# Kernel tuning notes

Measured on AMD Instinct MI355X. Metric: run time of the kernel, lower is better.

## Reference

```python
import jax, jax.numpy as jnp
import numpy as np

N_NODES = 100000
N_EDGES = 3200000
IN_FEAT = 128


def gcn_conv(x, src, dst, W, b, num_nodes):
    # PyG GCNConv: h = x @ W, then symmetric-normalized aggregation with self-loops.
    h = x @ W  # [N, out]
    # add self loops
    loop = jnp.arange(num_nodes, dtype=src.dtype)
    s = jnp.concatenate([src, loop])
    d = jnp.concatenate([dst, loop])
    # degree over destination (col) with unit edge weights
    deg = jax.ops.segment_sum(jnp.ones_like(s, dtype=h.dtype), d, num_segments=num_nodes)
    dinv = jnp.where(deg > 0, jax.lax.rsqrt(deg), 0.0)
    norm = dinv[s] * dinv[d]  # [E+N]
    msg = norm[:, None] * h[s]  # gather source features, scale per edge
    out = jax.ops.segment_sum(msg, d, num_segments=num_nodes)
    return out + b


def setup_inputs() -> dict:
    key = jax.random.key(0)
    ks = jax.random.split(key, 8)
    x = jax.random.normal(ks[0], (N_NODES, IN_FEAT), dtype=jnp.float32)
    edge_index = jax.random.randint(ks[1], (2, N_EDGES), 0, N_NODES, dtype=jnp.int64)
    def glorot(k, shape):
        lim = np.sqrt(6.0 / (shape[0] + shape[1]))
        return jax.random.uniform(k, shape, jnp.float32, -lim, lim)
    return {
        "x": x,
        "edge_index": edge_index,
        "W1": glorot(ks[2], (IN_FEAT, 4)), "b1": jnp.zeros((4,), jnp.float32),
        "W2": glorot(ks[3], (4, 2)),       "b2": jnp.zeros((2,), jnp.float32),
        "W3": glorot(ks[4], (2, 1)),       "b3": jnp.zeros((1,), jnp.float32),
    }


def reference(x, edge_index, W1, b1, W2, b2, W3, b3):
    src, dst = edge_index[0], edge_index[1]
    n = x.shape[0]
    h = gcn_conv(x, src, dst, W1, b1, n)
    h = jax.nn.relu(h)
    # F.dropout(training=self.training): inference mode -> identity
    h = gcn_conv(h, src, dst, W2, b2, n)
    h = jax.nn.relu(h)
    h = gcn_conv(h, src, dst, W3, b3, n)
    return jax.nn.sigmoid(h)  # [N, 1]
```

## Files before the change

kernel.cpp:

```cpp
#include <hip/hip_runtime.h>
#include <math.h>


#define TPB 256
#define CHUNK 4096
#define EPT (CHUNK / TPB)
#define BSZ 128
#define SLAB2 4992
#define NSMAX 1024

__global__ __launch_bounds__(TPB) void k_part(
    const int* __restrict__ src, const int* __restrict__ dst,
    unsigned int* __restrict__ slab, int* __restrict__ lstartT,
    const float* __restrict__ x, const float* __restrict__ W1,
    float* __restrict__ h1,
    int NB, int NS, int E, int N)
{
    __shared__ int hist[NSMAX];
    __shared__ unsigned int sorted[CHUNK];
    __shared__ int wtot[4];
    int t = threadIdx.x;

    if (blockIdx.x >= NS) {
        float* Ws = (float*)sorted;
        for (int i = t; i < 512; i += TPB) Ws[i] = W1[i];
        __syncthreads();
        int tt = (blockIdx.x - NS) * TPB + t;
        int v = tt >> 2, p = tt & 3;
        if (v >= N) return;
        const float4* xr = (const float4*)(x + (size_t)v * 128);
        float a0 = 0.f, a1 = 0.f, a2 = 0.f, a3 = 0.f;
#pragma unroll
        for (int i = 0; i < 8; ++i) {
            int cc = p + i * 4;
            float4 xx = xr[cc];
            const float* wv = &Ws[cc * 16];
            a0 += xx.x*wv[0] + xx.y*wv[4] + xx.z*wv[8]  + xx.w*wv[12];
            a1 += xx.x*wv[1] + xx.y*wv[5] + xx.z*wv[9]  + xx.w*wv[13];
            a2 += xx.x*wv[2] + xx.y*wv[6] + xx.z*wv[10] + xx.w*wv[14];
            a3 += xx.x*wv[3] + xx.y*wv[7] + xx.z*wv[11] + xx.w*wv[15];
        }
        a0 += __shfl_xor(a0,1); a0 += __shfl_xor(a0,2);
        a1 += __shfl_xor(a1,1); a1 += __shfl_xor(a1,2);
        a2 += __shfl_xor(a2,1); a2 += __shfl_xor(a2,2);
        a3 += __shfl_xor(a3,1); a3 += __shfl_xor(a3,2);
        if (p == 0) ((float4*)h1)[v] = make_float4(a0, a1, a2, a3);
        return;
    }

    int base = blockIdx.x * CHUNK;
    int n = min(CHUNK, E - base);
    for (int i = t; i < NSMAX; i += TPB) hist[i] = 0;
    __syncthreads();
    unsigned int meta[EPT];
#pragma unroll
    for (int k = 0; k < EPT; ++k) {
        int li = k * TPB + t;
        if (li < n) {
            int d = dst[base + li];
            int lp = atomicAdd(&hist[d >> 7], 1);
            meta[k] = ((unsigned)d << 13) | (unsigned)lp;
        } else meta[k] = 0xFFFFFFFFu;
    }
    __syncthreads();
    int lane = t & 63, w = t >> 6;
    int q0 = hist[4*t], q1 = hist[4*t+1], q2 = hist[4*t+2], q3 = hist[4*t+3];
    int pq = q0 + q1 + q2 + q3, xs = pq;
    for (int d = 1; d < 64; d <<= 1) { int y = __shfl_up(xs, d); if (lane >= d) xs += y; }
    if (lane == 63) wtot[w] = xs;
    __syncthreads();
    int woff = 0;
#pragma unroll
    for (int i = 0; i < 4; ++i) if (i < w) woff += wtot[i];
    int e0 = woff + xs - pq;
    hist[4*t]   = e0;
    hist[4*t+1] = e0 + q0;
    hist[4*t+2] = e0 + q0 + q1;
    hist[4*t+3] = e0 + q0 + q1 + q2;
    __syncthreads();
#pragma unroll
    for (int k = 0; k < EPT; ++k) {
        if (meta[k] != 0xFFFFFFFFu) {
            unsigned m = meta[k];
            int d = (int)(m >> 13);
            int lp = (int)(m & 0x1FFFu);
            unsigned pk = (unsigned)src[base + k*TPB + t] | ((unsigned)(d & 127) << 17);
            sorted[hist[d >> 7] + lp] = pk;
        }
    }
    __syncthreads();
    const uint4* s4 = (const uint4*)sorted;
    uint4* g4 = (uint4*)(slab + (size_t)base);
    for (int i = t; i < CHUNK / 4; i += TPB) g4[i] = s4[i];
    for (int i = t; i < NB + 1; i += TPB)
        lstartT[(size_t)i * NS + blockIdx.x] = hist[i];
}

__global__ __launch_bounds__(TPB) void k_degree(
    const unsigned int* __restrict__ slab, const int* __restrict__ lstartT,
    int* __restrict__ ssrc, int2* __restrict__ oc, float* __restrict__ dinv,
    const float* __restrict__ h1, float* __restrict__ hs1,
    int NS, int NB, int N)
{
    __shared__ unsigned int pl[SLAB2];
    __shared__ int sstart[NSMAX];
    __shared__ int slen[NSMAX];
    __shared__ int c[BSZ];
    __shared__ int cur[BSZ];
    __shared__ int wtot[4];
    int t = threadIdx.x, b = blockIdx.x;
    if (t < BSZ) c[t] = 0;
    for (int j = t; j < NSMAX; j += TPB) {
        int st = 0, len = 0;
        if (j < NS) {
            st  = lstartT[(size_t)b * NS + j];
            len = lstartT[(size_t)(b + 1) * NS + j] - st;
        }
        sstart[j] = st;
        slen[j] = len;
    }
    __syncthreads();
    int lane = t & 63, w = t >> 6;
    int s0 = slen[4*t], s1 = slen[4*t+1], s2 = slen[4*t+2], s3 = slen[4*t+3];
    int pq = s0 + s1 + s2 + s3, xs = pq;
    for (int d = 1; d < 64; d <<= 1) { int y = __shfl_up(xs, d); if (lane >= d) xs += y; }
    if (lane == 63) wtot[w] = xs;
    __syncthreads();
    int woff = 0, tot = 0;
#pragma unroll
    for (int i = 0; i < 4; ++i) { int z = wtot[i]; tot += z; if (i < w) woff += z; }
    int e0 = woff + xs - pq;
    slen[4*t]   = e0;
    slen[4*t+1] = e0 + s0;
    slen[4*t+2] = e0 + s0 + s1;
    slen[4*t+3] = e0 + s0 + s1 + s2;
    __syncthreads();
    int total = min(tot, SLAB2);
    for (int i = t; i < total; i += TPB) {
        int lo = 0, hi = NS;
        while (hi - lo > 1) {
            int mid = (lo + hi) >> 1;
            bool le = (slen[mid] <= i);
            lo = le ? mid : lo;
            hi = le ? hi : mid;
        }
        pl[i] = slab[(size_t)lo * CHUNK + sstart[lo] + (i - slen[lo])];
    }
    __syncthreads();
    for (int i = t; i < total; i += TPB) atomicAdd(&c[(pl[i] >> 17) & 127], 1);
    __syncthreads();
    int cv = (t < BSZ) ? c[t] : 0;
    int xc = cv;
    for (int d = 1; d < 64; d <<= 1) { int y = __shfl_up(xc, d); if (lane >= d) xc += y; }
    if (lane == 63) wtot[w] = xc;
    __syncthreads();
    int woff2 = 0;
#pragma unroll
    for (int i = 0; i < 4; ++i) if (i < w) woff2 += wtot[i];
    int excl = woff2 + xc - cv;
    if (t < BSZ) {
        int v = (b << 7) + t;
        if (v < N) {
            oc[v] = make_int2(b * SLAB2 + excl, cv);
            float di = rsqrtf((float)(cv + 1));
            dinv[v] = di;
            float4 hv = ((const float4*)h1)[v];
            ((float4*)hs1)[v] = make_float4(di*hv.x, di*hv.y, di*hv.z, di*hv.w);
        }
        cur[t] = excl;
    }
    __syncthreads();
    int* sb = ssrc + (size_t)b * SLAB2;
    for (int i = t; i < total; i += TPB) {
        unsigned pk = pl[i];
        int pos = atomicAdd(&cur[(pk >> 17) & 127], 1);
        sb[pos] = (int)(pk & 0x1FFFFu);
    }
}

__global__ __launch_bounds__(TPB) void k_gather1(
    const int2* __restrict__ oc, const int* __restrict__ ssrc,
    const float* __restrict__ hs1, const float* __restrict__ dinv,
    const float* __restrict__ b1, const float* __restrict__ W2,
    float* __restrict__ hs2, int n) {
    int t = blockIdx.x * TPB + threadIdx.x;
    int v = t >> 3, p = t & 7;
    if (v >= n) return;
    int2 ocv = oc[v];
    int base = ocv.x, c = ocv.y;
    float4 acc = make_float4(0.f, 0.f, 0.f, 0.f);
    for (int i = p; i < c; i += 8) {
        int s = ssrc[base + i];
        float4 h = ((const float4*)hs1)[s];
        acc.x += h.x; acc.y += h.y; acc.z += h.z; acc.w += h.w;
    }
    acc.x += __shfl_xor(acc.x, 1); acc.x += __shfl_xor(acc.x, 2); acc.x += __shfl_xor(acc.x, 4);
    acc.y += __shfl_xor(acc.y, 1); acc.y += __shfl_xor(acc.y, 2); acc.y += __shfl_xor(acc.y, 4);
    acc.z += __shfl_xor(acc.z, 1); acc.z += __shfl_xor(acc.z, 2); acc.z += __shfl_xor(acc.z, 4);
    acc.w += __shfl_xor(acc.w, 1); acc.w += __shfl_xor(acc.w, 2); acc.w += __shfl_xor(acc.w, 4);
    if (p == 0) {
        float4 hv = ((const float4*)hs1)[v];
        float di = dinv[v];
        float o0 = fmaxf(di * (acc.x + hv.x) + b1[0], 0.f);
        float o1 = fmaxf(di * (acc.y + hv.y) + b1[1], 0.f);
        float o2 = fmaxf(di * (acc.z + hv.z) + b1[2], 0.f);
        float o3 = fmaxf(di * (acc.w + hv.w) + b1[3], 0.f);
        float g0 = o0 * W2[0] + o1 * W2[2] + o2 * W2[4] + o3 * W2[6];
        float g1 = o0 * W2[1] + o1 * W2[3] + o2 * W2[5] + o3 * W2[7];
        ((float2*)hs2)[v] = make_float2(di * g0, di * g1);
    }
}

__global__ __launch_bounds__(TPB) void k_gather2(
    const int2* __restrict__ oc, const int* __restrict__ ssrc,
    const float* __restrict__ hs2, const float* __restrict__ dinv,
    const float* __restrict__ b2, const float* __restrict__ W3,
    float* __restrict__ hs3, int n) {
    int t = blockIdx.x * TPB + threadIdx.x;
    int v = t >> 3, p = t & 7;
    if (v >= n) return;
    int2 ocv = oc[v];
    int base = ocv.x, c = ocv.y;
    float2 acc = make_float2(0.f, 0.f);
    for (int i = p; i < c; i += 8) {
        int s = ssrc[base + i];
        float2 h = ((const float2*)hs2)[s];
        acc.x += h.x; acc.y += h.y;
    }
    acc.x += __shfl_xor(acc.x, 1); acc.x += __shfl_xor(acc.x, 2); acc.x += __shfl_xor(acc.x, 4);
    acc.y += __shfl_xor(acc.y, 1); acc.y += __shfl_xor(acc.y, 2); acc.y += __shfl_xor(acc.y, 4);
    if (p == 0) {
        float2 hv = ((const float2*)hs2)[v];
        float di = dinv[v];
        float o0 = fmaxf(di * (acc.x + hv.x) + b2[0], 0.f);
        float o1 = fmaxf(di * (acc.y + hv.y) + b2[1], 0.f);
        float h3 = o0 * W3[0] + o1 * W3[1];
        hs3[v] = di * h3;
    }
}

__global__ __launch_bounds__(TPB) void k_gather3(
    const int2* __restrict__ oc, const int* __restrict__ ssrc,
    const float* __restrict__ hs3, const float* __restrict__ dinv,
    const float* __restrict__ b3, float* __restrict__ out, int n) {
    int t = blockIdx.x * TPB + threadIdx.x;
    int v = t >> 3, p = t & 7;
    if (v >= n) return;
    int2 ocv = oc[v];
    int base = ocv.x, c = ocv.y;
    float acc = 0.f;
    for (int i = p; i < c; i += 8) acc += hs3[ssrc[base + i]];
    acc += __shfl_xor(acc, 1); acc += __shfl_xor(acc, 2); acc += __shfl_xor(acc, 4);
    if (p == 0) {
        float di = dinv[v];
        float agg = di * (acc + hs3[v]) + b3[0];
        out[v] = 1.0f / (1.0f + __expf(-agg));
    }
}

extern "C" void kernel_launch(void* const* d_in, const int* in_sizes, int n_in,
                              void* d_out, int out_size, void* d_ws, size_t ws_size,
                              hipStream_t stream) {
    const float* x  = (const float*)d_in[0];
    const int* ei   = (const int*)d_in[1];
    const float* W1 = (const float*)d_in[2];
    const float* b1 = (const float*)d_in[3];
    const float* W2 = (const float*)d_in[4];
    const float* b2 = (const float*)d_in[5];
    const float* W3 = (const float*)d_in[6];
    const float* b3 = (const float*)d_in[7];
    float* out = (float*)d_out;

    const int N = in_sizes[0] / 128;
    const int E = in_sizes[1] / 2;
    const int* src = ei;
    const int* dst = ei + E;

    const int NS = (E + CHUNK - 1) / CHUNK;
    const int NB = (N + BSZ - 1) / BSZ;

    char* w = (char*)d_ws;
    auto carve = [&](size_t bytes) { char* p = w; w += (bytes + 15) & ~(size_t)15; return p; };
    unsigned int* slab = (unsigned int*)carve((size_t)NS * CHUNK * 4);
    int* lstartT       = (int*)carve((size_t)(NB + 1) * NS * 4);
    int* ssrc          = (int*)carve((size_t)NB * SLAB2 * 4);
    int2* oc           = (int2*)carve((size_t)N * 8);
    float* dinv        = (float*)carve((size_t)N * 4);
    float* h1          = (float*)carve((size_t)4 * N * 4);
    float* hs1         = (float*)carve((size_t)4 * N * 4);
    float* hs2         = (float*)carve((size_t)2 * N * 4);
    float* hs3         = (float*)carve((size_t)N * 4);

    const int nb1  = (4 * N + TPB - 1) / TPB;
    const int nbN8 = (8 * N + TPB - 1) / TPB;

    k_part   <<<NS + nb1, TPB, 0, stream>>>(src, dst, slab, lstartT, x, W1, h1, NB, NS, E, N);
    k_degree <<<NB, TPB, 0, stream>>>(slab, lstartT, ssrc, oc, dinv, h1, hs1, NS, NB, N);
    k_gather1<<<nbN8, TPB, 0, stream>>>(oc, ssrc, hs1, dinv, b1, W2, hs2, N);
    k_gather2<<<nbN8, TPB, 0, stream>>>(oc, ssrc, hs2, dinv, b2, W3, hs3, N);
    k_gather3<<<nbN8, TPB, 0, stream>>>(oc, ssrc, hs3, dinv, b3, out, N);
}
```

Measured before the change: 217.7 us.

## Compute degrees with global atomics and fuse layer-1 gather into bucket build

Result: slower. 335.4 us (+54.0%).

```diff
diff --git a/kernel.cpp b/kernel.cpp
--- a/kernel.cpp
+++ b/kernel.cpp
@@ -9,9 +9,15 @@
 #define SLAB2 4992
 #define NSMAX 1024
 
+__global__ __launch_bounds__(TPB) void k_zero(int* __restrict__ deg, int n4) {
+    int i = blockIdx.x * TPB + threadIdx.x;
+    if (i < n4) ((int4*)deg)[i] = make_int4(0, 0, 0, 0);
+}
+
 __global__ __launch_bounds__(TPB) void k_part(
     const int* __restrict__ src, const int* __restrict__ dst,
     unsigned int* __restrict__ slab, int* __restrict__ lstartT,
+    int* __restrict__ deg,
     const float* __restrict__ x, const float* __restrict__ W1,
     float* __restrict__ h1,
     int NB, int NS, int E, int N)
@@ -58,6 +64,7 @@
         int li = k * TPB + t;
         if (li < n) {
             int d = dst[base + li];
+            atomicAdd(&deg[d], 1);
             int lp = atomicAdd(&hist[d >> 7], 1);
             meta[k] = ((unsigned)d << 13) | (unsigned)lp;
         } else meta[k] = 0xFFFFFFFFu;
@@ -96,20 +103,48 @@
         lstartT[(size_t)i * NS + blockIdx.x] = hist[i];
 }
 
-__global__ __launch_bounds__(TPB) void k_degree(
+__global__ __launch_bounds__(TPB) void k_dinv(
+    const int* __restrict__ deg, const float* __restrict__ h1,
+    float* __restrict__ dinv, float* __restrict__ hs1,
+    int2* __restrict__ oc, int N)
+{
+    __shared__ int wt[4];
+    int t = threadIdx.x;
+    int v = blockIdx.x * TPB + t;
+    int dg = (v < N) ? deg[v] : 0;
+    int lane = t & 63, w = t >> 6;
+    int xc = dg;
+    for (int d = 1; d < 64; d <<= 1) { int y = __shfl_up(xc, d); if (lane >= d) xc += y; }
+    if (lane == 63) wt[w] = xc;
+    __syncthreads();
+    int excl = xc - dg + ((w & 1) ? wt[w - 1] : 0);
+    if (v < N) {
+        int b = v >> 7;
+        oc[v] = make_int2(b * SLAB2 + excl, dg);
+        float di = rsqrtf((float)(dg + 1));
+        dinv[v] = di;
+        float4 hv = ((const float4*)h1)[v];
+        ((float4*)hs1)[v] = make_float4(di*hv.x, di*hv.y, di*hv.z, di*hv.w);
+    }
+}
+
+__global__ __launch_bounds__(TPB) void k_deg_g1(
     const unsigned int* __restrict__ slab, const int* __restrict__ lstartT,
-    int* __restrict__ ssrc, int2* __restrict__ oc, float* __restrict__ dinv,
-    const float* __restrict__ h1, float* __restrict__ hs1,
+    int* __restrict__ ssrc, const int2* __restrict__ oc,
+    const float* __restrict__ hs1, const float* __restrict__ dinv,
+    const float* __restrict__ b1, const float* __restrict__ W2,
+    float* __restrict__ hs2,
     int NS, int NB, int N)
 {
     __shared__ unsigned int pl[SLAB2];
     __shared__ int sstart[NSMAX];
     __shared__ int slen[NSMAX];
-    __shared__ int c[BSZ];
+    __shared__ int excl0[BSZ];
+    __shared__ int cnt0[BSZ];
     __shared__ int cur[BSZ];
     __shared__ int wtot[4];
     int t = threadIdx.x, b = blockIdx.x;
-    if (t < BSZ) c[t] = 0;
+
     for (int j = t; j < NSMAX; j += TPB) {
         int st = 0, len = 0;
         if (j < NS) {
@@ -118,6 +153,12 @@
         }
         sstart[j] = st;
         slen[j] = len;
+    }
+    if (t < BSZ) {
+        int v = (b << 7) + t;
+        int2 o = (v < N) ? oc[v] : make_int2(b * SLAB2, 0);
+        int e = o.x - b * SLAB2;
+        excl0[t] = e; cnt0[t] = o.y; cur[t] = e;
     }
     __syncthreads();
     int lane = t & 63, w = t >> 6;
@@ -136,38 +177,18 @@
     slen[4*t+3] = e0 + s0 + s1 + s2;
     __syncthreads();
     int total = min(tot, SLAB2);
-    for (int i = t; i < total; i += TPB) {
-        int lo = 0, hi = NS;
-        while (hi - lo > 1) {
-            int mid = (lo + hi) >> 1;
-            bool le = (slen[mid] <= i);
-            lo = le ? mid : lo;
-            hi = le ? hi : mid;
-        }
-        pl[i] = slab[(size_t)lo * CHUNK + sstart[lo] + (i - slen[lo])];
-    }
-    __syncthreads();
-    for (int i = t; i < total; i += TPB) atomicAdd(&c[(pl[i] >> 17) & 127], 1);
-    __syncthreads();
-    int cv = (t < BSZ) ? c[t] : 0;
-    int xc = cv;
-    for (int d = 1; d < 64; d <<= 1) { int y = __shfl_up(xc, d); if (lane >= d) xc += y; }
-    if (lane == 63) wtot[w] = xc;
-    __syncthreads();
-    int woff2 = 0;
-#pragma unroll
-    for (int i = 0; i < 4; ++i) if (i < w) woff2 += wtot[i];
-    int excl = woff2 + xc - cv;
-    if (t < BSZ) {
-        int v = (b << 7) + t;
-        if (v < N) {
-            oc[v] = make_int2(b * SLAB2 + excl, cv);
-            float di = rsqrtf((float)(cv + 1));
-            dinv[v] = di;
-            float4 hv = ((const float4*)h1)[v];
-            ((float4*)hs1)[v] = make_float4(di*hv.x, di*hv.y, di*hv.z, di*hv.w);
-        }
-        cur[t] = excl;
+    for (int i0 = t; i0 < total; i0 += 2*TPB) {
+        int i1 = i0 + TPB;
+        bool has1 = (i1 < total);
+        int lo0 = 0, lo1 = 0;
+#pragma unroll
+        for (int s = 512; s > 0; s >>= 1) {
+            if (slen[lo0 + s] <= i0) lo0 += s;
+            if (has1 && slen[lo1 + s] <= i1) lo1 += s;
+        }
+        pl[i0] = slab[(size_t)lo0 * CHUNK + sstart[lo0] + (i0 - slen[lo0])];
+        if (has1)
+            pl[i1] = slab[(size_t)lo1 * CHUNK + sstart[lo1] + (i1 - slen[lo1])];
     }
     __syncthreads();
     int* sb = ssrc + (size_t)b * SLAB2;
@@ -176,38 +197,43 @@
         int pos = atomicAdd(&cur[(pk >> 17) & 127], 1);
         sb[pos] = (int)(pk & 0x1FFFFu);
     }
-}
-
-__global__ __launch_bounds__(TPB) void k_gather1(
-    const int2* __restrict__ oc, const int* __restrict__ ssrc,
-    const float* __restrict__ hs1, const float* __restrict__ dinv,
-    const float* __restrict__ b1, const float* __restrict__ W2,
-    float* __restrict__ hs2, int n) {
-    int t = blockIdx.x * TPB + threadIdx.x;
-    int v = t >> 3, p = t & 7;
-    if (v >= n) return;
-    int2 ocv = oc[v];
-    int base = ocv.x, c = ocv.y;
-    float4 acc = make_float4(0.f, 0.f, 0.f, 0.f);
-    for (int i = p; i < c; i += 8) {
-        int s = ssrc[base + i];
-        float4 h = ((const float4*)hs1)[s];
-        acc.x += h.x; acc.y += h.y; acc.z += h.z; acc.w += h.w;
-    }
-    acc.x += __shfl_xor(acc.x, 1); acc.x += __shfl_xor(acc.x, 2); acc.x += __shfl_xor(acc.x, 4);
-    acc.y += __shfl_xor(acc.y, 1); acc.y += __shfl_xor(acc.y, 2); acc.y += __shfl_xor(acc.y, 4);
-    acc.z += __shfl_xor(acc.z, 1); acc.z += __shfl_xor(acc.z, 2); acc.z += __shfl_xor(acc.z, 4);
-    acc.w += __shfl_xor(acc.w, 1); acc.w += __shfl_xor(acc.w, 2); acc.w += __shfl_xor(acc.w, 4);
-    if (p == 0) {
-        float4 hv = ((const float4*)hs1)[v];
-        float di = dinv[v];
-        float o0 = fmaxf(di * (acc.x + hv.x) + b1[0], 0.f);
-        float o1 = fmaxf(di * (acc.y + hv.y) + b1[1], 0.f);
-        float o2 = fmaxf(di * (acc.z + hv.z) + b1[2], 0.f);
-        float o3 = fmaxf(di * (acc.w + hv.w) + b1[3], 0.f);
-        float g0 = o0 * W2[0] + o1 * W2[2] + o2 * W2[4] + o3 * W2[6];
-        float g1 = o0 * W2[1] + o1 * W2[3] + o2 * W2[5] + o3 * W2[7];
-        ((float2*)hs2)[v] = make_float2(di * g0, di * g1);
+    __syncthreads();
+    const float4* H = (const float4*)hs1;
+#pragma unroll
+    for (int ps = 0; ps < 4; ++ps) {
+        int vl = ps * 32 + (t >> 3);
+        int p = t & 7;
+        int v = (b << 7) + vl;
+        int c = cnt0[vl];
+        int b0 = excl0[vl];
+        float4 acc = make_float4(0.f, 0.f, 0.f, 0.f);
+        for (int i = p; i < c; i += 32) {
+            bool m1 = (i + 8 < c), m2 = (i + 16 < c), m3 = (i + 24 < c);
+            int s0v = sb[b0 + i];
+            int s1v = sb[b0 + (m1 ? i + 8  : i)];
+            int s2v = sb[b0 + (m2 ? i + 16 : i)];
+            int s3v = sb[b0 + (m3 ? i + 24 : i)];
+            float4 h0 = H[s0v], h1v = H[s1v], h2 = H[s2v], h3 = H[s3v];
+            acc.x += h0.x; acc.y += h0.y; acc.z += h0.z; acc.w += h0.w;
+            if (m1) { acc.x += h1v.x; acc.y += h1v.y; acc.z += h1v.z; acc.w += h1v.w; }
+            if (m2) { acc.x += h2.x;  acc.y += h2.y;  acc.z += h2.z;  acc.w += h2.w; }
+            if (m3) { acc.x += h3.x;  acc.y += h3.y;  acc.z += h3.z;  acc.w += h3.w; }
+        }
+        acc.x += __shfl_xor(acc.x,1); acc.x += __shfl_xor(acc.x,2); acc.x += __shfl_xor(acc.x,4);
+        acc.y += __shfl_xor(acc.y,1); acc.y += __shfl_xor(acc.y,2); acc.y += __shfl_xor(acc.y,4);
+        acc.z += __shfl_xor(acc.z,1); acc.z += __shfl_xor(acc.z,2); acc.z += __shfl_xor(acc.z,4);
+        acc.w += __shfl_xor(acc.w,1); acc.w += __shfl_xor(acc.w,2); acc.w += __shfl_xor(acc.w,4);
+        if (p == 0 && v < N) {
+            float4 hv = H[v];
+            float di = dinv[v];
+            float o0 = fmaxf(di * (acc.x + hv.x) + b1[0], 0.f);
+            float o1 = fmaxf(di * (acc.y + hv.y) + b1[1], 0.f);
+            float o2 = fmaxf(di * (acc.z + hv.z) + b1[2], 0.f);
+            float o3 = fmaxf(di * (acc.w + hv.w) + b1[3], 0.f);
+            float g0 = o0 * W2[0] + o1 * W2[2] + o2 * W2[4] + o3 * W2[6];
+            float g1 = o0 * W2[1] + o1 * W2[3] + o2 * W2[5] + o3 * W2[7];
+            ((float2*)hs2)[v] = make_float2(di * g0, di * g1);
+        }
     }
 }
 
@@ -221,21 +247,29 @@
     if (v >= n) return;
     int2 ocv = oc[v];
     int base = ocv.x, c = ocv.y;
+    const float2* H = (const float2*)hs2;
     float2 acc = make_float2(0.f, 0.f);
-    for (int i = p; i < c; i += 8) {
-        int s = ssrc[base + i];
-        float2 h = ((const float2*)hs2)[s];
-        acc.x += h.x; acc.y += h.y;
-    }
-    acc.x += __shfl_xor(acc.x, 1); acc.x += __shfl_xor(acc.x, 2); acc.x += __shfl_xor(acc.x, 4);
-    acc.y += __shfl_xor(acc.y, 1); acc.y += __shfl_xor(acc.y, 2); acc.y += __shfl_xor(acc.y, 4);
+    for (int i = p; i < c; i += 32) {
+        bool m1 = (i + 8 < c), m2 = (i + 16 < c), m3 = (i + 24 < c);
+        int s0 = ssrc[base + i];
+        int s1 = ssrc[base + (m1 ? i + 8  : i)];
+        int s2 = ssrc[base + (m2 ? i + 16 : i)];
+        int s3 = ssrc[base + (m3 ? i + 24 : i)];
+        float2 h0 = H[s0], h1 = H[s1], h2 = H[s2], h3 = H[s3];
+        acc.x += h0.x; acc.y += h0.y;
+        if (m1) { acc.x += h1.x; acc.y += h1.y; }
+        if (m2) { acc.x += h2.x; acc.y += h2.y; }
+        if (m3) { acc.x += h3.x; acc.y += h3.y; }
+    }
+    acc.x += __shfl_xor(acc.x,1); acc.x += __shfl_xor(acc.x,2); acc.x += __shfl_xor(acc.x,4);
+    acc.y += __shfl_xor(acc.y,1); acc.y += __shfl_xor(acc.y,2); acc.y += __shfl_xor(acc.y,4);
     if (p == 0) {
-        float2 hv = ((const float2*)hs2)[v];
+        float2 hv = H[v];
         float di = dinv[v];
         float o0 = fmaxf(di * (acc.x + hv.x) + b2[0], 0.f);
         float o1 = fmaxf(di * (acc.y + hv.y) + b2[1], 0.f);
-        float h3 = o0 * W3[0] + o1 * W3[1];
-        hs3[v] = di * h3;
+        float h3v = o0 * W3[0] + o1 * W3[1];
+        hs3[v] = di * h3v;
     }
 }
 
@@ -249,7 +283,18 @@
     int2 ocv = oc[v];
     int base = ocv.x, c = ocv.y;
     float acc = 0.f;
-    for (int i = p; i < c; i += 8) acc += hs3[ssrc[base + i]];
+    for (int i = p; i < c; i += 32) {
+        bool m1 = (i + 8 < c), m2 = (i + 16 < c), m3 = (i + 24 < c);
+        int s0 = ssrc[base + i];
+        int s1 = ssrc[base + (m1 ? i + 8  : i)];
+        int s2 = ssrc[base + (m2 ? i + 16 : i)];
+        int s3 = ssrc[base + (m3 ? i + 24 : i)];
+        float h0 = hs3[s0], h1 = hs3[s1], h2 = hs3[s2], h3 = hs3[s3];
+        acc += h0;
+        if (m1) acc += h1;
+        if (m2) acc += h2;
+        if (m3) acc += h3;
+    }
     acc += __shfl_xor(acc, 1); acc += __shfl_xor(acc, 2); acc += __shfl_xor(acc, 4);
     if (p == 0) {
         float di = dinv[v];
@@ -283,20 +328,25 @@
     auto carve = [&](size_t bytes) { char* p = w; w += (bytes + 15) & ~(size_t)15; return p; };
     unsigned int* slab = (unsigned int*)carve((size_t)NS * CHUNK * 4);
     int* lstartT       = (int*)carve((size_t)(NB + 1) * NS * 4);
-    int* ssrc          = (int*)carve((size_t)NB * SLAB2 * 4);
+    int* ssrc          = (int*)carve((size_t)NB * SLAB2 * 4 + 128);
     int2* oc           = (int2*)carve((size_t)N * 8);
+    int* deg           = (int*)carve((size_t)((N + 3) & ~3) * 4);
     float* dinv        = (float*)carve((size_t)N * 4);
     float* h1          = (float*)carve((size_t)4 * N * 4);
     float* hs1         = (float*)carve((size_t)4 * N * 4);
     float* hs2         = (float*)carve((size_t)2 * N * 4);
     float* hs3         = (float*)carve((size_t)N * 4);
 
+    const int n4   = (N + 3) / 4;
+    const int nbz  = (n4 + TPB - 1) / TPB;
     const int nb1  = (4 * N + TPB - 1) / TPB;
+    const int nbN  = (N + TPB - 1) / TPB;
     const int nbN8 = (8 * N + TPB - 1) / TPB;
 
-    k_part   <<<NS + nb1, TPB, 0, stream>>>(src, dst, slab, lstartT, x, W1, h1, NB, NS, E, N);
-    k_degree <<<NB, TPB, 0, stream>>>(slab, lstartT, ssrc, oc, dinv, h1, hs1, NS, NB, N);
-    k_gather1<<<nbN8, TPB, 0, stream>>>(oc, ssrc, hs1, dinv, b1, W2, hs2, N);
+    k_zero   <<<nbz, TPB, 0, stream>>>(deg, n4);
+    k_part   <<<NS + nb1, TPB, 0, stream>>>(src, dst, slab, lstartT, deg, x, W1, h1, NB, NS, E, N);
+    k_dinv   <<<nbN, TPB, 0, stream>>>(deg, h1, dinv, hs1, oc, N);
+    k_deg_g1 <<<NB, TPB, 0, stream>>>(slab, lstartT, ssrc, oc, hs1, dinv, b1, W2, hs2, NS, NB, N);
     k_gather2<<<nbN8, TPB, 0, stream>>>(oc, ssrc, hs2, dinv, b2, W3, hs3, N);
     k_gather3<<<nbN8, TPB, 0, stream>>>(oc, ssrc, hs3, dinv, b3, out, N);
 }
```

## Replace per-node CSR sort with per-bucket packed edges and LDS atomic aggregation

Applied to the files above, without the earlier changes.

New measurement: 306.4 us. +40.7%, slower.

```diff
diff --git a/kernel.cpp b/kernel.cpp
--- a/kernel.cpp
+++ b/kernel.cpp
@@ -96,17 +96,16 @@
         lstartT[(size_t)i * NS + blockIdx.x] = hist[i];
 }
 
-__global__ __launch_bounds__(TPB) void k_degree(
+__global__ __launch_bounds__(TPB) void k_merge(
     const unsigned int* __restrict__ slab, const int* __restrict__ lstartT,
-    int* __restrict__ ssrc, int2* __restrict__ oc, float* __restrict__ dinv,
-    const float* __restrict__ h1, float* __restrict__ hs1,
+    unsigned int* __restrict__ pkd, int* __restrict__ bcnt,
+    const float* __restrict__ h1, float* __restrict__ dinv, float* __restrict__ hs1,
     int NS, int NB, int N)
 {
     __shared__ unsigned int pl[SLAB2];
     __shared__ int sstart[NSMAX];
     __shared__ int slen[NSMAX];
     __shared__ int c[BSZ];
-    __shared__ int cur[BSZ];
     __shared__ int wtot[4];
     int t = threadIdx.x, b = blockIdx.x;
     if (t < BSZ) c[t] = 0;
@@ -136,125 +135,138 @@
     slen[4*t+3] = e0 + s0 + s1 + s2;
     __syncthreads();
     int total = min(tot, SLAB2);
-    for (int i = t; i < total; i += TPB) {
-        int lo = 0, hi = NS;
-        while (hi - lo > 1) {
-            int mid = (lo + hi) >> 1;
-            bool le = (slen[mid] <= i);
-            lo = le ? mid : lo;
-            hi = le ? hi : mid;
-        }
-        pl[i] = slab[(size_t)lo * CHUNK + sstart[lo] + (i - slen[lo])];
-    }
-    __syncthreads();
-    for (int i = t; i < total; i += TPB) atomicAdd(&c[(pl[i] >> 17) & 127], 1);
-    __syncthreads();
-    int cv = (t < BSZ) ? c[t] : 0;
-    int xc = cv;
-    for (int d = 1; d < 64; d <<= 1) { int y = __shfl_up(xc, d); if (lane >= d) xc += y; }
-    if (lane == 63) wtot[w] = xc;
-    __syncthreads();
-    int woff2 = 0;
-#pragma unroll
-    for (int i = 0; i < 4; ++i) if (i < w) woff2 += wtot[i];
-    int excl = woff2 + xc - cv;
+    int per = ((total + TPB - 1) / TPB) | 1;
+    int i0 = t * per, i1 = min(i0 + per, total);
+    if (i0 < i1) {
+        int lo = 0;
+#pragma unroll
+        for (int s = 512; s > 0; s >>= 1)
+            if (slen[lo + s] <= i0) lo += s;
+        for (int i = i0; i < i1; ++i) {
+            while (slen[lo + 1] <= i) ++lo;
+            unsigned v = slab[(size_t)lo * CHUNK + sstart[lo] + (i - slen[lo])];
+            pl[i] = v;
+            atomicAdd(&c[(v >> 17) & 127], 1);
+        }
+    }
+    __syncthreads();
+    int n4 = (total + 3) >> 2;
+    const uint4* p4 = (const uint4*)pl;
+    uint4* g4 = (uint4*)(pkd + (size_t)b * SLAB2);
+    for (int i = t; i < n4; i += TPB) g4[i] = p4[i];
     if (t < BSZ) {
         int v = (b << 7) + t;
         if (v < N) {
-            oc[v] = make_int2(b * SLAB2 + excl, cv);
-            float di = rsqrtf((float)(cv + 1));
+            int dg = c[t];
+            float di = rsqrtf((float)(dg + 1));
             dinv[v] = di;
             float4 hv = ((const float4*)h1)[v];
             ((float4*)hs1)[v] = make_float4(di*hv.x, di*hv.y, di*hv.z, di*hv.w);
         }
-        cur[t] = excl;
-    }
-    __syncthreads();
-    int* sb = ssrc + (size_t)b * SLAB2;
-    for (int i = t; i < total; i += TPB) {
-        unsigned pk = pl[i];
-        int pos = atomicAdd(&cur[(pk >> 17) & 127], 1);
-        sb[pos] = (int)(pk & 0x1FFFFu);
-    }
-}
-
-__global__ __launch_bounds__(TPB) void k_gather1(
-    const int2* __restrict__ oc, const int* __restrict__ ssrc,
+    }
+    if (t == 0) bcnt[b] = total;
+}
+
+__global__ __launch_bounds__(TPB) void k_g1(
+    const unsigned int* __restrict__ pkd, const int* __restrict__ bcnt,
     const float* __restrict__ hs1, const float* __restrict__ dinv,
     const float* __restrict__ b1, const float* __restrict__ W2,
-    float* __restrict__ hs2, int n) {
-    int t = blockIdx.x * TPB + threadIdx.x;
-    int v = t >> 3, p = t & 7;
-    if (v >= n) return;
-    int2 ocv = oc[v];
-    int base = ocv.x, c = ocv.y;
-    float4 acc = make_float4(0.f, 0.f, 0.f, 0.f);
-    for (int i = p; i < c; i += 8) {
-        int s = ssrc[base + i];
-        float4 h = ((const float4*)hs1)[s];
-        acc.x += h.x; acc.y += h.y; acc.z += h.z; acc.w += h.w;
-    }
-    acc.x += __shfl_xor(acc.x, 1); acc.x += __shfl_xor(acc.x, 2); acc.x += __shfl_xor(acc.x, 4);
-    acc.y += __shfl_xor(acc.y, 1); acc.y += __shfl_xor(acc.y, 2); acc.y += __shfl_xor(acc.y, 4);
-    acc.z += __shfl_xor(acc.z, 1); acc.z += __shfl_xor(acc.z, 2); acc.z += __shfl_xor(acc.z, 4);
-    acc.w += __shfl_xor(acc.w, 1); acc.w += __shfl_xor(acc.w, 2); acc.w += __shfl_xor(acc.w, 4);
-    if (p == 0) {
-        float4 hv = ((const float4*)hs1)[v];
-        float di = dinv[v];
-        float o0 = fmaxf(di * (acc.x + hv.x) + b1[0], 0.f);
-        float o1 = fmaxf(di * (acc.y + hv.y) + b1[1], 0.f);
-        float o2 = fmaxf(di * (acc.z + hv.z) + b1[2], 0.f);
-        float o3 = fmaxf(di * (acc.w + hv.w) + b1[3], 0.f);
-        float g0 = o0 * W2[0] + o1 * W2[2] + o2 * W2[4] + o3 * W2[6];
-        float g1 = o0 * W2[1] + o1 * W2[3] + o2 * W2[5] + o3 * W2[7];
-        ((float2*)hs2)[v] = make_float2(di * g0, di * g1);
-    }
-}
-
-__global__ __launch_bounds__(TPB) void k_gather2(
-    const int2* __restrict__ oc, const int* __restrict__ ssrc,
+    float* __restrict__ hs2, int N)
+{
+    __shared__ float acc[BSZ][4];
+    int t = threadIdx.x, b = blockIdx.x;
+    if (t < BSZ) { acc[t][0] = 0.f; acc[t][1] = 0.f; acc[t][2] = 0.f; acc[t][3] = 0.f; }
+    __syncthreads();
+    int total = bcnt[b];
+    const unsigned int* pb = pkd + (size_t)b * SLAB2;
+    const float4* H = (const float4*)hs1;
+#pragma unroll 4
+    for (int i = t; i < total; i += TPB) {
+        unsigned p = pb[i];
+        int s = (int)(p & 0x1FFFFu), dl = (int)((p >> 17) & 127u);
+        float4 h = H[s];
+        atomicAdd(&acc[dl][0], h.x);
+        atomicAdd(&acc[dl][1], h.y);
+        atomicAdd(&acc[dl][2], h.z);
+        atomicAdd(&acc[dl][3], h.w);
+    }
+    __syncthreads();
+    if (t < BSZ) {
+        int v = (b << 7) + t;
+        if (v < N) {
+            float4 hv = H[v];
+            float di = dinv[v];
+            float o0 = fmaxf(di * (acc[t][0] + hv.x) + b1[0], 0.f);
+            float o1 = fmaxf(di * (acc[t][1] + hv.y) + b1[1], 0.f);
+            float o2 = fmaxf(di * (acc[t][2] + hv.z) + b1[2], 0.f);
+            float o3 = fmaxf(di * (acc[t][3] + hv.w) + b1[3], 0.f);
+            float g0 = o0 * W2[0] + o1 * W2[2] + o2 * W2[4] + o3 * W2[6];
+            float g1 = o0 * W2[1] + o1 * W2[3] + o2 * W2[5] + o3 * W2[7];
+            ((float2*)hs2)[v] = make_float2(di * g0, di * g1);
+        }
+    }
+}
+
+__global__ __launch_bounds__(TPB) void k_g2(
+    const unsigned int* __restrict__ pkd, const int* __restrict__ bcnt,
     const float* __restrict__ hs2, const float* __restrict__ dinv,
     const float* __restrict__ b2, const float* __restrict__ W3,
-    float* __restrict__ hs3, int n) {
-    int t = blockIdx.x * TPB + threadIdx.x;
-    int v = t >> 3, p = t & 7;
-    if (v >= n) return;
-    int2 ocv = oc[v];
-    int base = ocv.x, c = ocv.y;
-    float2 acc = make_float2(0.f, 0.f);
-    for (int i = p; i < c; i += 8) {
-        int s = ssrc[base + i];
-        float2 h = ((const float2*)hs2)[s];
-        acc.x += h.x; acc.y += h.y;
-    }
-    acc.x += __shfl_xor(acc.x, 1); acc.x += __shfl_xor(acc.x, 2); acc.x += __shfl_xor(acc.x, 4);
-    acc.y += __shfl_xor(acc.y, 1); acc.y += __shfl_xor(acc.y, 2); acc.y += __shfl_xor(acc.y, 4);
-    if (p == 0) {
-        float2 hv = ((const float2*)hs2)[v];
-        float di = dinv[v];
-        float o0 = fmaxf(di * (acc.x + hv.x) + b2[0], 0.f);
-        float o1 = fmaxf(di * (acc.y + hv.y) + b2[1], 0.f);
-        float h3 = o0 * W3[0] + o1 * W3[1];
-        hs3[v] = di * h3;
-    }
-}
-
-__global__ __launch_bounds__(TPB) void k_gather3(
-    const int2* __restrict__ oc, const int* __restrict__ ssrc,
+    float* __restrict__ hs3, int N)
+{
+    __shared__ float acc[BSZ][2];
+    int t = threadIdx.x, b = blockIdx.x;
+    if (t < BSZ) { acc[t][0] = 0.f; acc[t][1] = 0.f; }
+    __syncthreads();
+    int total = bcnt[b];
+    const unsigned int* pb = pkd + (size_t)b * SLAB2;
+    const float2* H = (const float2*)hs2;
+#pragma unroll 4
+    for (int i = t; i < total; i += TPB) {
+        unsigned p = pb[i];
+        int s = (int)(p & 0x1FFFFu), dl = (int)((p >> 17) & 127u);
+        float2 h = H[s];
+        atomicAdd(&acc[dl][0], h.x);
+        atomicAdd(&acc[dl][1], h.y);
+    }
+    __syncthreads();
+    if (t < BSZ) {
+        int v = (b << 7) + t;
+        if (v < N) {
+            float2 hv = H[v];
+            float di = dinv[v];
+            float o0 = fmaxf(di * (acc[t][0] + hv.x) + b2[0], 0.f);
+            float o1 = fmaxf(di * (acc[t][1] + hv.y) + b2[1], 0.f);
+            float h3v = o0 * W3[0] + o1 * W3[1];
+            hs3[v] = di * h3v;
+        }
+    }
+}
+
+__global__ __launch_bounds__(TPB) void k_g3(
+    const unsigned int* __restrict__ pkd, const int* __restrict__ bcnt,
     const float* __restrict__ hs3, const float* __restrict__ dinv,
-    const float* __restrict__ b3, float* __restrict__ out, int n) {
-    int t = blockIdx.x * TPB + threadIdx.x;
-    int v = t >> 3, p = t & 7;
-    if (v >= n) return;
-    int2 ocv = oc[v];
-    int base = ocv.x, c = ocv.y;
-    float acc = 0.f;
-    for (int i = p; i < c; i += 8) acc += hs3[ssrc[base + i]];
-    acc += __shfl_xor(acc, 1); acc += __shfl_xor(acc, 2); acc += __shfl_xor(acc, 4);
-    if (p == 0) {
-        float di = dinv[v];
-        float agg = di * (acc + hs3[v]) + b3[0];
-        out[v] = 1.0f / (1.0f + __expf(-agg));
+    const float* __restrict__ b3, float* __restrict__ out, int N)
+{
+    __shared__ float acc[BSZ];
+    int t = threadIdx.x, b = blockIdx.x;
+    if (t < BSZ) acc[t] = 0.f;
+    __syncthreads();
+    int total = bcnt[b];
+    const unsigned int* pb = pkd + (size_t)b * SLAB2;
+#pragma unroll 4
+    for (int i = t; i < total; i += TPB) {
+        unsigned p = pb[i];
+        int s = (int)(p & 0x1FFFFu), dl = (int)((p >> 17) & 127u);
+        atomicAdd(&acc[dl], hs3[s]);
+    }
+    __syncthreads();
+    if (t < BSZ) {
+        int v = (b << 7) + t;
+        if (v < N) {
+            float di = dinv[v];
+            float agg = di * (acc[t] + hs3[v]) + b3[0];
+            out[v] = 1.0f / (1.0f + __expf(-agg));
+        }
     }
 }
 
@@ -283,20 +295,19 @@
     auto carve = [&](size_t bytes) { char* p = w; w += (bytes + 15) & ~(size_t)15; return p; };
     unsigned int* slab = (unsigned int*)carve((size_t)NS * CHUNK * 4);
     int* lstartT       = (int*)carve((size_t)(NB + 1) * NS * 4);
-    int* ssrc          = (int*)carve((size_t)NB * SLAB2 * 4);
-    int2* oc           = (int2*)carve((size_t)N * 8);
+    unsigned int* pkd  = (unsigned int*)carve((size_t)NB * SLAB2 * 4);
+    int* bcnt          = (int*)carve((size_t)NB * 4);
     float* dinv        = (float*)carve((size_t)N * 4);
     float* h1          = (float*)carve((size_t)4 * N * 4);
     float* hs1         = (float*)carve((size_t)4 * N * 4);
     float* hs2         = (float*)carve((size_t)2 * N * 4);
     float* hs3         = (float*)carve((size_t)N * 4);
 
-    const int nb1  = (4 * N + TPB - 1) / TPB;
-    const int nbN8 = (8 * N + TPB - 1) / TPB;
-
-    k_part   <<<NS + nb1, TPB, 0, stream>>>(src, dst, slab, lstartT, x, W1, h1, NB, NS, E, N);
-    k_degree <<<NB, TPB, 0, stream>>>(slab, lstartT, ssrc, oc, dinv, h1, hs1, NS, NB, N);
-    k_gather1<<<nbN8, TPB, 0, stream>>>(oc, ssrc, hs1, dinv, b1, W2, hs2, N);
-    k_gather2<<<nbN8, TPB, 0, stream>>>(oc, ssrc, hs2, dinv, b2, W3, hs3, N);
-    k_gather3<<<nbN8, TPB, 0, stream>>>(oc, ssrc, hs3, dinv, b3, out, N);
-}
+    const int nb1 = (4 * N + TPB - 1) / TPB;
+
+    k_part <<<NS + nb1, TPB, 0, stream>>>(src, dst, slab, lstartT, x, W1, h1, NB, NS, E, N);
+    k_merge<<<NB, TPB, 0, stream>>>(slab, lstartT, pkd, bcnt, h1, dinv, hs1, NS, NB, N);
+    k_g1   <<<NB, TPB, 0, stream>>>(pkd, bcnt, hs1, dinv, b1, W2, hs2, N);
+    k_g2   <<<NB, TPB, 0, stream>>>(pkd, bcnt, hs2, dinv, b2, W3, hs3, N);
+    k_g3   <<<NB, TPB, 0, stream>>>(pkd, bcnt, hs3, dinv, b3, out, N);
+}
```

## Scatter partitioned edges directly into per-bucket slabs via global atomics and unroll gathers

Applied to the files above, without the earlier changes.

Result: slower. 258.0 us (+18.5%).

```diff
diff --git a/kernel.cpp b/kernel.cpp
--- a/kernel.cpp
+++ b/kernel.cpp
@@ -11,13 +11,14 @@
 
 __global__ __launch_bounds__(TPB) void k_part(
     const int* __restrict__ src, const int* __restrict__ dst,
-    unsigned int* __restrict__ slab, int* __restrict__ lstartT,
+    unsigned int* __restrict__ ebuf, int* __restrict__ bktCnt,
     const float* __restrict__ x, const float* __restrict__ W1,
     float* __restrict__ h1,
     int NB, int NS, int E, int N)
 {
     __shared__ int hist[NSMAX];
     __shared__ unsigned int sorted[CHUNK];
+    __shared__ unsigned short binof[CHUNK];
     __shared__ int wtot[4];
     int t = threadIdx.x;
 
@@ -73,10 +74,17 @@
 #pragma unroll
     for (int i = 0; i < 4; ++i) if (i < w) woff += wtot[i];
     int e0 = woff + xs - pq;
-    hist[4*t]   = e0;
-    hist[4*t+1] = e0 + q0;
-    hist[4*t+2] = e0 + q0 + q1;
-    hist[4*t+3] = e0 + q0 + q1 + q2;
+    int ex0 = e0, ex1 = e0 + q0, ex2 = e0 + q0 + q1, ex3 = e0 + q0 + q1 + q2;
+    int bin0 = 4 * t;
+    int g0 = 0, g1v = 0, g2v = 0, g3v = 0;
+    if (q0 > 0 && bin0 + 0 < NB) g0  = atomicAdd(&bktCnt[bin0 + 0], q0);
+    if (q1 > 0 && bin0 + 1 < NB) g1v = atomicAdd(&bktCnt[bin0 + 1], q1);
+    if (q2 > 0 && bin0 + 2 < NB) g2v = atomicAdd(&bktCnt[bin0 + 2], q2);
+    if (q3 > 0 && bin0 + 3 < NB) g3v = atomicAdd(&bktCnt[bin0 + 3], q3);
+    hist[4*t]   = ex0 | (min(g0,  8191) << 13);
+    hist[4*t+1] = ex1 | (min(g1v, 8191) << 13);
+    hist[4*t+2] = ex2 | (min(g2v, 8191) << 13);
+    hist[4*t+3] = ex3 | (min(g3v, 8191) << 13);
     __syncthreads();
 #pragma unroll
     for (int k = 0; k < EPT; ++k) {
@@ -84,71 +92,42 @@
             unsigned m = meta[k];
             int d = (int)(m >> 13);
             int lp = (int)(m & 0x1FFFu);
-            unsigned pk = (unsigned)src[base + k*TPB + t] | ((unsigned)(d & 127) << 17);
-            sorted[hist[d >> 7] + lp] = pk;
+            int bin = d >> 7;
+            int pos = (hist[bin] & 0x1FFF) + lp;
+            sorted[pos] = (unsigned)src[base + k*TPB + t] | ((unsigned)(d & 127) << 17);
+            binof[pos] = (unsigned short)bin;
         }
     }
     __syncthreads();
-    const uint4* s4 = (const uint4*)sorted;
-    uint4* g4 = (uint4*)(slab + (size_t)base);
-    for (int i = t; i < CHUNK / 4; i += TPB) g4[i] = s4[i];
-    for (int i = t; i < NB + 1; i += TPB)
-        lstartT[(size_t)i * NS + blockIdx.x] = hist[i];
-}
-
-__global__ __launch_bounds__(TPB) void k_degree(
-    const unsigned int* __restrict__ slab, const int* __restrict__ lstartT,
+    for (int p = t; p < n; p += TPB) {
+        int bin = binof[p];
+        int combo = hist[bin];
+        int dp = (combo >> 13) + (p - (combo & 0x1FFF));
+        if (dp < SLAB2)
+            ebuf[(size_t)bin * SLAB2 + dp] = sorted[p];
+    }
+}
+
+__global__ __launch_bounds__(TPB) void k_merge(
+    const unsigned int* __restrict__ ebuf, const int* __restrict__ bktCnt,
     int* __restrict__ ssrc, int2* __restrict__ oc, float* __restrict__ dinv,
-    const float* __restrict__ h1, float* __restrict__ hs1,
-    int NS, int NB, int N)
+    const float* __restrict__ h1, float* __restrict__ hs1, int NB, int N)
 {
     __shared__ unsigned int pl[SLAB2];
-    __shared__ int sstart[NSMAX];
-    __shared__ int slen[NSMAX];
     __shared__ int c[BSZ];
     __shared__ int cur[BSZ];
     __shared__ int wtot[4];
     int t = threadIdx.x, b = blockIdx.x;
     if (t < BSZ) c[t] = 0;
-    for (int j = t; j < NSMAX; j += TPB) {
-        int st = 0, len = 0;
-        if (j < NS) {
-            st  = lstartT[(size_t)b * NS + j];
-            len = lstartT[(size_t)(b + 1) * NS + j] - st;
-        }
-        sstart[j] = st;
-        slen[j] = len;
-    }
+    int total = min(bktCnt[b], SLAB2);
+    const uint4* e4 = (const uint4*)(ebuf + (size_t)b * SLAB2);
+    uint4* p4 = (uint4*)pl;
+    int n4 = (total + 3) >> 2;
+    for (int i = t; i < n4; i += TPB) p4[i] = e4[i];
+    __syncthreads();
+    for (int i = t; i < total; i += TPB) atomicAdd(&c[(pl[i] >> 17) & 127], 1);
     __syncthreads();
     int lane = t & 63, w = t >> 6;
-    int s0 = slen[4*t], s1 = slen[4*t+1], s2 = slen[4*t+2], s3 = slen[4*t+3];
-    int pq = s0 + s1 + s2 + s3, xs = pq;
-    for (int d = 1; d < 64; d <<= 1) { int y = __shfl_up(xs, d); if (lane >= d) xs += y; }
-    if (lane == 63) wtot[w] = xs;
-    __syncthreads();
-    int woff = 0, tot = 0;
-#pragma unroll
-    for (int i = 0; i < 4; ++i) { int z = wtot[i]; tot += z; if (i < w) woff += z; }
-    int e0 = woff + xs - pq;
-    slen[4*t]   = e0;
-    slen[4*t+1] = e0 + s0;
-    slen[4*t+2] = e0 + s0 + s1;
-    slen[4*t+3] = e0 + s0 + s1 + s2;
-    __syncthreads();
-    int total = min(tot, SLAB2);
-    for (int i = t; i < total; i += TPB) {
-        int lo = 0, hi = NS;
-        while (hi - lo > 1) {
-            int mid = (lo + hi) >> 1;
-            bool le = (slen[mid] <= i);
-            lo = le ? mid : lo;
-            hi = le ? hi : mid;
-        }
-        pl[i] = slab[(size_t)lo * CHUNK + sstart[lo] + (i - slen[lo])];
-    }
-    __syncthreads();
-    for (int i = t; i < total; i += TPB) atomicAdd(&c[(pl[i] >> 17) & 127], 1);
-    __syncthreads();
     int cv = (t < BSZ) ? c[t] : 0;
     int xc = cv;
     for (int d = 1; d < 64; d <<= 1) { int y = __shfl_up(xc, d); if (lane >= d) xc += y; }
@@ -188,18 +167,26 @@
     if (v >= n) return;
     int2 ocv = oc[v];
     int base = ocv.x, c = ocv.y;
+    const float4* H = (const float4*)hs1;
     float4 acc = make_float4(0.f, 0.f, 0.f, 0.f);
-    for (int i = p; i < c; i += 8) {
-        int s = ssrc[base + i];
-        float4 h = ((const float4*)hs1)[s];
-        acc.x += h.x; acc.y += h.y; acc.z += h.z; acc.w += h.w;
-    }
-    acc.x += __shfl_xor(acc.x, 1); acc.x += __shfl_xor(acc.x, 2); acc.x += __shfl_xor(acc.x, 4);
-    acc.y += __shfl_xor(acc.y, 1); acc.y += __shfl_xor(acc.y, 2); acc.y += __shfl_xor(acc.y, 4);
-    acc.z += __shfl_xor(acc.z, 1); acc.z += __shfl_xor(acc.z, 2); acc.z += __shfl_xor(acc.z, 4);
-    acc.w += __shfl_xor(acc.w, 1); acc.w += __shfl_xor(acc.w, 2); acc.w += __shfl_xor(acc.w, 4);
+    for (int i = p; i < c; i += 32) {
+        bool m1 = (i + 8 < c), m2 = (i + 16 < c), m3 = (i + 24 < c);
+        int s0 = ssrc[base + i];
+        int s1 = ssrc[base + (m1 ? i + 8  : i)];
+        int s2 = ssrc[base + (m2 ? i + 16 : i)];
+        int s3 = ssrc[base + (m3 ? i + 24 : i)];
+        float4 h0 = H[s0], h1v = H[s1], h2 = H[s2], h3 = H[s3];
+        acc.x += h0.x; acc.y += h0.y; acc.z += h0.z; acc.w += h0.w;
+        if (m1) { acc.x += h1v.x; acc.y += h1v.y; acc.z += h1v.z; acc.w += h1v.w; }
+        if (m2) { acc.x += h2.x;  acc.y += h2.y;  acc.z += h2.z;  acc.w += h2.w; }
+        if (m3) { acc.x += h3.x;  acc.y += h3.y;  acc.z += h3.z;  acc.w += h3.w; }
+    }
+    acc.x += __shfl_xor(acc.x,1); acc.x += __shfl_xor(acc.x,2); acc.x += __shfl_xor(acc.x,4);
+    acc.y += __shfl_xor(acc.y,1); acc.y += __shfl_xor(acc.y,2); acc.y += __shfl_xor(acc.y,4);
+    acc.z += __shfl_xor(acc.z,1); acc.z += __shfl_xor(acc.z,2); acc.z += __shfl_xor(acc.z,4);
+    acc.w += __shfl_xor(acc.w,1); acc.w += __shfl_xor(acc.w,2); acc.w += __shfl_xor(acc.w,4);
     if (p == 0) {
-        float4 hv = ((const float4*)hs1)[v];
+        float4 hv = H[v];
         float di = dinv[v];
         float o0 = fmaxf(di * (acc.x + hv.x) + b1[0], 0.f);
         float o1 = fmaxf(di * (acc.y + hv.y) + b1[1], 0.f);
@@ -221,21 +208,29 @@
     if (v >= n) return;
     int2 ocv = oc[v];
     int base = ocv.x, c = ocv.y;
+    const float2* H = (const float2*)hs2;
     float2 acc = make_float2(0.f, 0.f);
-    for (int i = p; i < c; i += 8) {
-        int s = ssrc[base + i];
-        float2 h = ((const float2*)hs2)[s];
-        acc.x += h.x; acc.y += h.y;
-    }
-    acc.x += __shfl_xor(acc.x, 1); acc.x += __shfl_xor(acc.x, 2); acc.x += __shfl_xor(acc.x, 4);
-    acc.y += __shfl_xor(acc.y, 1); acc.y += __shfl_xor(acc.y, 2); acc.y += __shfl_xor(acc.y, 4);
+    for (int i = p; i < c; i += 32) {
+        bool m1 = (i + 8 < c), m2 = (i + 16 < c), m3 = (i + 24 < c);
+        int s0 = ssrc[base + i];
+        int s1 = ssrc[base + (m1 ? i + 8  : i)];
+        int s2 = ssrc[base + (m2 ? i + 16 : i)];
+        int s3 = ssrc[base + (m3 ? i + 24 : i)];
+        float2 h0 = H[s0], h1 = H[s1], h2 = H[s2], h3 = H[s3];
+        acc.x += h0.x; acc.y += h0.y;
+        if (m1) { acc.x += h1.x; acc.y += h1.y; }
+        if (m2) { acc.x += h2.x; acc.y += h2.y; }
+        if (m3) { acc.x += h3.x; acc.y += h3.y; }
+    }
+    acc.x += __shfl_xor(acc.x,1); acc.x += __shfl_xor(acc.x,2); acc.x += __shfl_xor(acc.x,4);
+    acc.y += __shfl_xor(acc.y,1); acc.y += __shfl_xor(acc.y,2); acc.y += __shfl_xor(acc.y,4);
     if (p == 0) {
-        float2 hv = ((const float2*)hs2)[v];
+        float2 hv = H[v];
         float di = dinv[v];
         float o0 = fmaxf(di * (acc.x + hv.x) + b2[0], 0.f);
         float o1 = fmaxf(di * (acc.y + hv.y) + b2[1], 0.f);
-        float h3 = o0 * W3[0] + o1 * W3[1];
-        hs3[v] = di * h3;
+        float h3v = o0 * W3[0] + o1 * W3[1];
+        hs3[v] = di * h3v;
     }
 }
 
@@ -249,7 +244,18 @@
     int2 ocv = oc[v];
     int base = ocv.x, c = ocv.y;
     float acc = 0.f;
-    for (int i = p; i < c; i += 8) acc += hs3[ssrc[base + i]];
+    for (int i = p; i < c; i += 32) {
+        bool m1 = (i + 8 < c), m2 = (i + 16 < c), m3 = (i + 24 < c);
+        int s0 = ssrc[base + i];
+        int s1 = ssrc[base + (m1 ? i + 8  : i)];
+        int s2 = ssrc[base + (m2 ? i + 16 : i)];
+        int s3 = ssrc[base + (m3 ? i + 24 : i)];
+        float h0 = hs3[s0], h1 = hs3[s1], h2 = hs3[s2], h3 = hs3[s3];
+        acc += h0;
+        if (m1) acc += h1;
+        if (m2) acc += h2;
+        if (m3) acc += h3;
+    }
     acc += __shfl_xor(acc, 1); acc += __shfl_xor(acc, 2); acc += __shfl_xor(acc, 4);
     if (p == 0) {
         float di = dinv[v];
@@ -281,9 +287,9 @@
 
     char* w = (char*)d_ws;
     auto carve = [&](size_t bytes) { char* p = w; w += (bytes + 15) & ~(size_t)15; return p; };
-    unsigned int* slab = (unsigned int*)carve((size_t)NS * CHUNK * 4);
-    int* lstartT       = (int*)carve((size_t)(NB + 1) * NS * 4);
-    int* ssrc          = (int*)carve((size_t)NB * SLAB2 * 4);
+    unsigned int* ebuf = (unsigned int*)carve((size_t)NB * SLAB2 * 4);
+    int* bktCnt        = (int*)carve((size_t)NB * 4);
+    int* ssrc          = (int*)carve((size_t)NB * SLAB2 * 4 + 128);
     int2* oc           = (int2*)carve((size_t)N * 8);
     float* dinv        = (float*)carve((size_t)N * 4);
     float* h1          = (float*)carve((size_t)4 * N * 4);
@@ -294,8 +300,9 @@
     const int nb1  = (4 * N + TPB - 1) / TPB;
     const int nbN8 = (8 * N + TPB - 1) / TPB;
 
-    k_part   <<<NS + nb1, TPB, 0, stream>>>(src, dst, slab, lstartT, x, W1, h1, NB, NS, E, N);
-    k_degree <<<NB, TPB, 0, stream>>>(slab, lstartT, ssrc, oc, dinv, h1, hs1, NS, NB, N);
+    hipMemsetAsync(bktCnt, 0, (size_t)NB * 4, stream);
+    k_part   <<<NS + nb1, TPB, 0, stream>>>(src, dst, ebuf, bktCnt, x, W1, h1, NB, NS, E, N);
+    k_merge  <<<NB, TPB, 0, stream>>>(ebuf, bktCnt, ssrc, oc, dinv, h1, hs1, NB, N);
     k_gather1<<<nbN8, TPB, 0, stream>>>(oc, ssrc, hs1, dinv, b1, W2, hs2, N);
     k_gather2<<<nbN8, TPB, 0, stream>>>(oc, ssrc, hs2, dinv, b2, W3, hs3, N);
     k_gather3<<<nbN8, TPB, 0, stream>>>(oc, ssrc, hs3, dinv, b3, out, N);
```
